# Kernel optimization log

Hardware: AMD Instinct MI355X
Metric: run time of the kernel (lower is better)

## Reference

```python
import jax, jax.numpy as jnp
import numpy as np

D_MODEL, H, D_FF = 512, 8, 2048
B, S = 2, 2048
EPS = 1e-6


def _layernorm(x, alpha, beta):
    # Faithful to the torch module: unbiased std (ddof=1), eps added to STD,
    # scalar alpha/beta parameters.
    m = jnp.mean(x, axis=-1, keepdims=True)
    var = jnp.sum((x - m) ** 2, axis=-1, keepdims=True) / (x.shape[-1] - 1)
    std = jnp.sqrt(var)
    return alpha * (x - m) / (std + EPS) + beta


def _mha(x, mask, Wq, bq, Wk, bk, Wv, bv, Wo, bo):
    Bn, Sn, D = x.shape
    dk = D // H
    q = (x @ Wq + bq).reshape(Bn, Sn, H, dk).transpose(0, 2, 1, 3)  # [B,H,S,dk]
    k = (x @ Wk + bk).reshape(Bn, Sn, H, dk).transpose(0, 2, 1, 3)
    v = (x @ Wv + bv).reshape(Bn, Sn, H, dk).transpose(0, 2, 1, 3)
    scores = jnp.einsum('bhqd,bhkd->bhqk', q, k) / jnp.sqrt(jnp.float32(dk))
    scores = jnp.where(mask == 0, -jnp.inf, scores)  # mask [B,1,1,S] broadcasts
    attn = jax.nn.softmax(scores, axis=-1)
    out = jnp.einsum('bhqk,bhkd->bhqd', attn, v)
    out = out.transpose(0, 2, 1, 3).reshape(Bn, Sn, D)
    return out @ Wo + bo


def _ffn(x, W1, b1, W2, b2):
    return jax.nn.relu(x @ W1 + b1) @ W2 + b2


def setup_inputs() -> dict:
    key = jax.random.key(0)
    ks = jax.random.split(key, 12)
    sd = 1.0 / np.sqrt(D_MODEL)
    sdf = 1.0 / np.sqrt(D_FF)
    inp = {
        'x': jax.random.normal(ks[0], (B, S, D_MODEL), jnp.float32),
        'src_mask': jnp.ones((B, 1, 1, S), jnp.int32),
        'Wq': jax.random.normal(ks[1], (D_MODEL, D_MODEL), jnp.float32) * sd,
        'bq': jnp.zeros((D_MODEL,), jnp.float32),
        'Wk': jax.random.normal(ks[2], (D_MODEL, D_MODEL), jnp.float32) * sd,
        'bk': jnp.zeros((D_MODEL,), jnp.float32),
        'Wv': jax.random.normal(ks[3], (D_MODEL, D_MODEL), jnp.float32) * sd,
        'bv': jnp.zeros((D_MODEL,), jnp.float32),
        'Wo': jax.random.normal(ks[4], (D_MODEL, D_MODEL), jnp.float32) * sd,
        'bo': jnp.zeros((D_MODEL,), jnp.float32),
        'W1': jax.random.normal(ks[5], (D_MODEL, D_FF), jnp.float32) * sd,
        'b1': jnp.zeros((D_FF,), jnp.float32),
        'W2': jax.random.normal(ks[6], (D_FF, D_MODEL), jnp.float32) * sdf,
        'b2': jnp.zeros((D_MODEL,), jnp.float32),
        'alpha1': jnp.ones((1,), jnp.float32),
        'beta1': jnp.zeros((1,), jnp.float32),
        'alpha2': jnp.ones((1,), jnp.float32),
        'beta2': jnp.zeros((1,), jnp.float32),
    }
    return inp


def reference(x, src_mask, Wq, bq, Wk, bk, Wv, bv, Wo, bo,
              W1, b1, W2, b2, alpha1, beta1, alpha2, beta2):
    # SkipConnection 0: x + dropout(MHA(LN(x)))  (dropout=0 -> identity)
    h1 = _layernorm(x, alpha1, beta1)
    x = x + _mha(h1, src_mask, Wq, bq, Wk, bk, Wv, bv, Wo, bo)
    # SkipConnection 1: x + dropout(FFN(LN(x)))
    h2 = _layernorm(x, alpha2, beta2)
    x = x + _ffn(h2, W1, b1, W2, b2)
    return x
```

## Files before the change

kernel.cpp:

```cpp
#include <hip/hip_runtime.h>
#include <hip/hip_bf16.h>

typedef __hip_bfloat16 bf16;
typedef __attribute__((ext_vector_type(8))) short s8v;
typedef __attribute__((ext_vector_type(4))) float f32x4;

#define DM 512
#define NH 8
#define DKH 64
#define DFF 2048
#define NB 2
#define NS 2048
#define NR (NB*NS)
#define LN_EPS 1e-6f
#define NEG_BIG (-1e30f)
#define LDQKV (3*DM)
#define SM_SHIFT (-6.0f)
#define PART_ELEMS (NB*NH*NS*DKH)

#define MFMA_B16(a,b,c) __builtin_amdgcn_mfma_f32_16x16x32_bf16(a,b,c,0,0,0)

#define GLOAD16(g, l) __builtin_amdgcn_global_load_lds( \
    (const __attribute__((address_space(1))) void*)(g), \
    (__attribute__((address_space(3))) void*)(l), 16, 0, 0)

__device__ __forceinline__ float us2f(unsigned int u){ return __uint_as_float(u << 16); }
__device__ __forceinline__ float b2f(bf16 v){ return __bfloat162float(v); }
__device__ __forceinline__ float ldf(const float* p){ return *p; }
__device__ __forceinline__ float ldf(const bf16* p){ return __bfloat162float(*p); }
__device__ __forceinline__ void stf(float* p, float v){ *p = v; }
__device__ __forceinline__ void stf(bf16* p, float v){ *p = __float2bfloat16(v); }
__device__ __forceinline__ unsigned short f2bu(float f){
  bf16 b = __float2bfloat16(f);
  return *reinterpret_cast<unsigned short*>(&b);
}

template<int N> __device__ __forceinline__ void waitcnt_vm(){
  if constexpr(N==0)      asm volatile("s_waitcnt vmcnt(0)" ::: "memory");
  else if constexpr(N==2) asm volatile("s_waitcnt vmcnt(2)" ::: "memory");
  else if constexpr(N==3) asm volatile("s_waitcnt vmcnt(3)" ::: "memory");
  else if constexpr(N==4) asm volatile("s_waitcnt vmcnt(4)" ::: "memory");
  else if constexpr(N==6) asm volatile("s_waitcnt vmcnt(6)" ::: "memory");
  else if constexpr(N==8) asm volatile("s_waitcnt vmcnt(8)" ::: "memory");
}

__device__ __forceinline__ int swz(int row, int colbyte){
  return ((row<<7) + colbyte) ^ ((row&7)<<4);
}

__device__ __forceinline__ float wsum(float v){
#pragma unroll
  for(int o=32;o>0;o>>=1) v += __shfl_down(v,o,64);
  return v;
}

__device__ __forceinline__ void stage_tile(char* lds, const bf16* g, int ld, int R, int tid){
  int wave = tid>>6, lane = tid&63;
  int nch = R*8;
  for(int c0 = wave*64; c0 < nch; c0 += 256){
    int c = c0 + lane;
    int row = c>>3;
    int blk = (c&7) ^ (row&7);
    GLOAD16(g + (size_t)row*ld + blk*8, lds + c0*16);
  }
}
__device__ __forceinline__ s8v read_frag(const char* lds, int row, int col){
  return *reinterpret_cast<const s8v*>(lds + swz(row, col<<1));
}

template<typename TI>
__global__ __launch_bounds__(256) void ln_kernel(const TI* __restrict__ x,
    bf16* __restrict__ out, const float* __restrict__ ap, const float* __restrict__ bp){
  __shared__ float s1[4], s2[4];
  int row = blockIdx.x, tid = threadIdx.x;
  const TI* xr = x + (size_t)row*DM;
  float v0 = ldf(xr+tid), v1 = ldf(xr+tid+256);
  float s = wsum(v0+v1);
  float q = wsum(v0*v0+v1*v1);
  int wid = tid>>6, lane = tid&63;
  if(lane==0){ s1[wid]=s; s2[wid]=q; }
  __syncthreads();
  float S = s1[0]+s1[1]+s1[2]+s1[3];
  float Q = s2[0]+s2[1]+s2[2]+s2[3];
  float mean = S*(1.f/DM);
  float var  = (Q - (float)DM*mean*mean)*(1.f/(DM-1));
  float sd   = sqrtf(fmaxf(var,0.f));
  float sc = (*ap)/(sd+LN_EPS);
  float b = *bp;
  bf16* orow = out + (size_t)row*DM;
  orow[tid]     = __float2bfloat16((v0-mean)*sc + b);
  orow[tid+256] = __float2bfloat16((v1-mean)*sc + b);
}

__global__ __launch_bounds__(256) void transpose_all(
    const float* __restrict__ Wq, const float* __restrict__ Wk,
    const float* __restrict__ Wv, const float* __restrict__ Wo,
    const float* __restrict__ W1, const float* __restrict__ W2,
    bf16* __restrict__ WTqkv, bf16* __restrict__ WTo,
    bf16* __restrict__ WT1, bf16* __restrict__ WT2){
  __shared__ float t[64][65];
  int tb = blockIdx.x;
  const float* W; bf16* WT; int K, N, nx;
  if(tb < 192){
    int w = tb>>6; tb &= 63;
    W = (w==0)?Wq:(w==1)?Wk:Wv; WT = WTqkv + w*512*512; K=512; N=512; nx=8;
  } else if(tb < 256){ tb -= 192; W=Wo; WT=WTo; K=512; N=512; nx=8; }
  else if(tb < 512){ tb -= 256; W=W1; WT=WT1; K=512; N=2048; nx=32; }
  else { tb -= 512; W=W2; WT=WT2; K=2048; N=512; nx=8; }
  int n0 = (tb % nx)*64, k0 = (tb / nx)*64;
  int tid = threadIdx.x;
  int rr = tid>>6, cc = tid&63;
#pragma unroll
  for(int r=rr;r<64;r+=4) t[r][cc] = W[(size_t)(k0+r)*N + n0+cc];
  __syncthreads();
#pragma unroll
  for(int r=rr;r<64;r+=4) WT[(size_t)(n0+r)*K + k0+cc] = __float2bfloat16(t[cc][r]);
}

__global__ __launch_bounds__(256) void transpose_v(const bf16* __restrict__ Vg,
    bf16* __restrict__ VT){
  __shared__ float t[64][65];
  int tid = threadIdx.x;
  int s0 = blockIdx.x*64; int bh = blockIdx.y;
  int b = bh>>3, h = bh&7;
  int rr = tid>>6, cc = tid&63;
#pragma unroll
  for(int r=rr;r<64;r+=4)
    t[r][cc] = b2f(Vg[((size_t)(b*NS + s0+r))*LDQKV + h*DKH + cc]);
  __syncthreads();
  int kp = (cc&15)*4 + (cc>>4);
#pragma unroll
  for(int r=rr;r<64;r+=4)
    VT[((size_t)bh*DKH + r)*NS + s0 + kp] = __float2bfloat16(t[cc][r]);
}

template<int BM, int BN, int RELU, int QKVSEL, typename TR, typename TO>
__global__ __launch_bounds__(256) void mfma_gemm(
    const bf16* __restrict__ A, const bf16* __restrict__ WT,
    const float* __restrict__ bias0, const float* __restrict__ bias1,
    const float* __restrict__ bias2,
    const TR* __restrict__ resid, TO* __restrict__ out, int M, int N, int K){
  constexpr int NW = BN/2, NF = NW/16, MI = (BM+31)/32, WRS = BM/2;
  constexpr int LOADS = BM/32 + BN/32;
  __shared__ char lA[2][BM*128];
  __shared__ char lB[2][BN*128];
  int tid = threadIdx.x, wave = tid>>6, lane = tid&63;
  int m0 = blockIdx.x*BM, n0 = blockIdx.y*BN;
  int wr = wave>>1, wc = wave&1;
  int g = lane>>4, li = lane&15;
  f32x4 acc[MI][NF] = {};
  stage_tile(lA[0], A + (size_t)m0*K, K, BM, tid);
  stage_tile(lB[0], WT + (size_t)n0*K, K, BN, tid);
  int NT = K>>6;
  int cur = 0;
  for(int t=0; t<NT; ++t, cur^=1){
    if(t+1 < NT){
      stage_tile(lA[cur^1], A + (size_t)m0*K + (t+1)*64, K, BM, tid);
      stage_tile(lB[cur^1], WT + (size_t)n0*K + (t+1)*64, K, BN, tid);
      waitcnt_vm<LOADS>();
    } else {
      waitcnt_vm<0>();
    }
    __builtin_amdgcn_sched_barrier(0);
    __builtin_amdgcn_s_barrier();
    __builtin_amdgcn_sched_barrier(0);
#pragma unroll
    for(int kk=0; kk<2; kk++){
      s8v af[MI], bfr[NF];
#pragma unroll
      for(int mi=0;mi<MI;mi++) af[mi] = read_frag(lA[cur], wr*WRS+mi*16+li, kk*32+g*8);
#pragma unroll
      for(int ni=0;ni<NF;ni++) bfr[ni] = read_frag(lB[cur], wc*NW+ni*16+li, kk*32+g*8);
#pragma unroll
      for(int mi=0;mi<MI;mi++)
#pragma unroll
        for(int ni=0;ni<NF;ni++)
          acc[mi][ni] = MFMA_B16(af[mi], bfr[ni], acc[mi][ni]);
    }
    __builtin_amdgcn_sched_barrier(0);
    __builtin_amdgcn_s_barrier();
  }
#pragma unroll
  for(int mi=0;mi<MI;mi++)
#pragma unroll
  for(int ni=0;ni<NF;ni++){
    int row = m0 + wr*WRS + mi*16 + g*4;
    int col = n0 + wc*NW + ni*16 + li;
    const float* bp = bias0;
    if(QKVSEL) bp = (col<512)? bias0 : (col<1024)? (bias1-512) : (bias2-1024);
    float bb = bp[col];
#pragma unroll
    for(int r=0;r<4;r++){
      float v = acc[mi][ni][r] + bb;
      if(RELU) v = fmaxf(v, 0.f);
      size_t off = (size_t)(row+r)*N + col;
      if(resid) v += ldf(resid+off);
      stf(out+off, v);
    }
  }
}

__global__ __launch_bounds__(256,4) void flash_attn(
    const bf16* __restrict__ QKV, const bf16* __restrict__ VT,
    const int* __restrict__ mask, bf16* __restrict__ partA,
    bf16* __restrict__ partB, float* __restrict__ lbuf){
  __shared__ char lK[2][64*128];
  __shared__ char lV[2][64*128];
  __shared__ char lP[4][16*128];
  int tid = threadIdx.x, wave = tid>>6, lane = tid&63;
  int bid = blockIdx.x;
  int xcd = bid & 7, u = bid >> 3;
  int q0 = (u & 31)*64;
  int bhk = xcd + 8*(u>>5);
  int h = bhk & 7, kh = (bhk>>3)&1, b = bhk>>4;
  int kbase = kh*(NS/2);
  int g = lane>>4, li = lane&15;
  const bf16* Qg  = QKV + ((size_t)b*NS + q0)*LDQKV + h*DKH;
  const bf16* Kg  = QKV + ((size_t)b*NS + kbase)*LDQKV + DM + h*DKH;
  const bf16* VTg = VT + ((size_t)(b*NH + h))*DKH*NS + kbase;
  stage_tile(lK[0], Qg, LDQKV, 64, tid);
  __syncthreads();
  s8v qf0 = read_frag(lK[0], wave*16+li, g*8);
  s8v qf1 = read_frag(lK[0], wave*16+li, 32+g*8);
  __syncthreads();
  stage_tile(lK[0], Kg, LDQKV, 64, tid);
  stage_tile(lV[0], VTg, NS, 64, tid);
  unsigned long long mb = 0;
#pragma unroll 16
  for(int j=0;j<64;j++)
    mb |= (unsigned long long)(mask[b*NS + kbase + j*16 + li] != 0) << j;
  __syncthreads();
  f32x4 acc[4] = {};
  f32x4 acc_l = {};
  s8v ones;
#pragma unroll
  for(int j=0;j<8;j++) ones[j] = (short)0x3F80;
  char* lPw = lP[wave];

  auto compute = [&](int kt, int c){
    f32x4 S[4] = {};
#pragma unroll
    for(int kk=0;kk<2;kk++){
      s8v qf = kk ? qf1 : qf0;
      s8v kf[4];
#pragma unroll
      for(int ni=0;ni<4;ni++) kf[ni] = read_frag(lK[c], ni*16+li, kk*32+g*8);
#pragma unroll
      for(int ni=0;ni<4;ni++)
        S[ni] = MFMA_B16(qf, kf[ni], S[ni]);
    }
    int jb = kt>>4;
    float madd[4];
#pragma unroll
    for(int ni=0;ni<4;ni++)
      madd[ni] = ((mb>>(jb+ni))&1ull) ? SM_SHIFT : NEG_BIG;
#pragma unroll
    for(int r=0;r<4;r++){
      float e0 = __expf(fmaf(S[0][r], 0.125f, madd[0]));
      float e1 = __expf(fmaf(S[1][r], 0.125f, madd[1]));
      float e2 = __expf(fmaf(S[2][r], 0.125f, madd[2]));
      float e3 = __expf(fmaf(S[3][r], 0.125f, madd[3]));
      int row = g*4 + r;
      uint2 w;
      w.x = (unsigned int)f2bu(e0) | ((unsigned int)f2bu(e1)<<16);
      w.y = (unsigned int)f2bu(e2) | ((unsigned int)f2bu(e3)<<16);
      *reinterpret_cast<uint2*>(lPw + swz(row, li<<3)) = w;
    }
#pragma unroll
    for(int kk=0;kk<2;kk++){
      s8v pf = read_frag(lPw, li, kk*32+g*8);
      s8v vf[4];
#pragma unroll
      for(int nd=0;nd<4;nd++) vf[nd] = read_frag(lV[c], nd*16+li, kk*32+g*8);
#pragma unroll
      for(int nd=0;nd<4;nd++)
        acc[nd] = MFMA_B16(pf, vf[nd], acc[nd]);
      acc_l = MFMA_B16(pf, ones, acc_l);
    }
  };

  int cur = 0;
  for(int t=0; t<15; ++t, cur^=1){
    stage_tile(lK[cur^1], Kg + (size_t)(t+1)*64*LDQKV, LDQKV, 64, tid);
    stage_tile(lV[cur^1], VTg + (t+1)*64, NS, 64, tid);
    waitcnt_vm<4>();
    __builtin_amdgcn_sched_barrier(0);
    __builtin_amdgcn_s_barrier();
    __builtin_amdgcn_sched_barrier(0);
    compute(t*64, cur);
    __builtin_amdgcn_sched_barrier(0);
    __builtin_amdgcn_s_barrier();
  }
  waitcnt_vm<0>();
  __builtin_amdgcn_sched_barrier(0);
  __builtin_amdgcn_s_barrier();
  __builtin_amdgcn_sched_barrier(0);
  compute(15*64, cur);

  bf16* part = kh ? partB : partA;
  size_t qb = (size_t)(b*NH + h)*NS;
#pragma unroll
  for(int r=0;r<4;r++){
    int qrow = q0 + wave*16 + g*4 + r;
#pragma unroll
    for(int nd=0;nd<4;nd++)
      part[(qb + qrow)*DKH + nd*16 + li] = __float2bfloat16(acc[nd][r]);
    if(li==0)
      lbuf[((size_t)((b*NH+h)*2 + kh))*NS + qrow] = acc_l[r];
  }
}

__global__ __launch_bounds__(256) void combine_attn(const bf16* __restrict__ pA,
    const bf16* __restrict__ pB, const float* __restrict__ lbuf,
    bf16* __restrict__ cx){
  int e = blockIdx.x*256 + threadIdx.x;
  int idx = e*4;
  int d = idx & 63, q = (idx>>6)&(NS-1), h = (idx>>17)&7, b = idx>>20;
  uint2 ua = *reinterpret_cast<const uint2*>(pA+idx);
  uint2 ub = *reinterpret_cast<const uint2*>(pB+idx);
  float lA = lbuf[((size_t)((b*NH+h)*2+0))*NS + q];
  float lB = lbuf[((size_t)((b*NH+h)*2+1))*NS + q];
  float il = 1.f/(lA+lB);
  bf16* o = cx + ((size_t)(b*NS+q)*DM + h*DKH + d);
  o[0] = __float2bfloat16((us2f(ua.x&0xffffu)+us2f(ub.x&0xffffu))*il);
  o[1] = __float2bfloat16((us2f(ua.x>>16)+us2f(ub.x>>16))*il);
  o[2] = __float2bfloat16((us2f(ua.y&0xffffu)+us2f(ub.y&0xffffu))*il);
  o[3] = __float2bfloat16((us2f(ua.y>>16)+us2f(ub.y>>16))*il);
}

extern "C" void kernel_launch(void* const* d_in, const int* in_sizes, int n_in,
                              void* d_out, int out_size, void* d_ws, size_t ws_size,
                              hipStream_t stream){
  const float* x   = (const float*)d_in[0];
  const int* mask  = (const int*)d_in[1];
  const float* Wq = (const float*)d_in[2];
  const float* bq = (const float*)d_in[3];
  const float* Wk = (const float*)d_in[4];
  const float* bk = (const float*)d_in[5];
  const float* Wv = (const float*)d_in[6];
  const float* bv = (const float*)d_in[7];
  const float* Wo = (const float*)d_in[8];
  const float* bo = (const float*)d_in[9];
  const float* W1 = (const float*)d_in[10];
  const float* b1 = (const float*)d_in[11];
  const float* W2 = (const float*)d_in[12];
  const float* b2 = (const float*)d_in[13];
  const float* a1 = (const float*)d_in[14];
  const float* be1= (const float*)d_in[15];
  const float* a2 = (const float*)d_in[16];
  const float* be2= (const float*)d_in[17];

  char* ws = (char*)d_ws;
  bf16* h1    = (bf16*)(ws);
  bf16* accA  = (bf16*)(ws);
  bf16* WTqkv = (bf16*)(ws + (size_t)( 4<<20));
  bf16* WTo   = (bf16*)(ws + (size_t)(11<<19));
  bf16* WT1   = (bf16*)(ws + (size_t)( 8<<20));
  bf16* WT2   = (bf16*)(ws + (size_t)(10<<20));
  bf16* qkv   = (bf16*)(ws + (size_t)(12<<20));
  bf16* VT    = (bf16*)(ws + (size_t)(24<<20));
  bf16* cx    = (bf16*)(ws + (size_t)(24<<20));
  bf16* x1    = h1;
  bf16* h2    = (bf16*)(ws + (size_t)( 4<<20));
  bf16* mid   = qkv;
  float* lbuf = (float*)d_out;
  bf16* accB  = (bf16*)((char*)d_out + (1<<20));

  transpose_all<<<768,256,0,stream>>>(Wq,Wk,Wv,Wo,W1,W2, WTqkv,WTo,WT1,WT2);

  ln_kernel<float><<<NR,256,0,stream>>>(x, h1, a1, be1);
  mfma_gemm<128,64,0,1,float,bf16><<<dim3(32,24),256,0,stream>>>(
      h1, WTqkv, bq, bk, bv, (const float*)nullptr, qkv, NR, LDQKV, DM);
  transpose_v<<<dim3(32,16),256,0,stream>>>(qkv + 2*DM, VT);
  flash_attn<<<1024,256,0,stream>>>(qkv, VT, mask, accA, accB, lbuf);
  combine_attn<<<PART_ELEMS/1024,256,0,stream>>>(accA, accB, lbuf, cx);
  mfma_gemm<32,64,0,0,float,bf16><<<dim3(128,8),256,0,stream>>>(
      cx, WTo, bo, bo, bo, x, x1, NR, DM, DM);
  ln_kernel<bf16><<<NR,256,0,stream>>>(x1, h2, a2, be2);
  mfma_gemm<128,128,1,0,float,bf16><<<dim3(32,16),256,0,stream>>>(
      h2, WT1, b1, b1, b1, (const float*)nullptr, mid, NR, DFF, DM);
  mfma_gemm<32,64,0,0,bf16,float><<<dim3(128,8),256,0,stream>>>(
      mid, WT2, b2, b2, b2, x1, (float*)d_out, NR, DM, DFF);
}
```

Measured before the change: 130.6 us.

## Use 128-query attention blocks with 8 waves sharing K/V tiles, add setprio

The flash attention kernel now runs 512 threads per block, each block covering 128 query rows instead of 64, so every staged K/V tile in LDS is reused by twice as many waves and the total K/V global traffic is halved. The Q tile is staged across both K buffers, the per-wave P scratch grows to 8 slots, and the wait count is adjusted for fewer loads per thread. s_setprio is raised around the MFMA sections so that waves doing matrix work are favoured over those doing the exp stage. The cost is half as many blocks (512) and larger blocks, which may lower occupancy or load balance across CUs.

Measured after the change: 127.1 us. 2.7% less time.

```diff
diff --git a/kernel.cpp b/kernel.cpp
--- a/kernel.cpp
+++ b/kernel.cpp
@@ -54,14 +54,13 @@
   return v;
 }
 
+template<int NTHR>
 __device__ __forceinline__ void stage_tile(char* lds, const bf16* g, int ld, int R, int tid){
-  int wave = tid>>6, lane = tid&63;
   int nch = R*8;
-  for(int c0 = wave*64; c0 < nch; c0 += 256){
-    int c = c0 + lane;
+  for(int c = tid; c < nch; c += NTHR){
     int row = c>>3;
     int blk = (c&7) ^ (row&7);
-    GLOAD16(g + (size_t)row*ld + blk*8, lds + c0*16);
+    GLOAD16(g + (size_t)row*ld + blk*8, lds + c*16);
   }
 }
 __device__ __forceinline__ s8v read_frag(const char* lds, int row, int col){
@@ -149,14 +148,14 @@
   int wr = wave>>1, wc = wave&1;
   int g = lane>>4, li = lane&15;
   f32x4 acc[MI][NF] = {};
-  stage_tile(lA[0], A + (size_t)m0*K, K, BM, tid);
-  stage_tile(lB[0], WT + (size_t)n0*K, K, BN, tid);
+  stage_tile<256>(lA[0], A + (size_t)m0*K, K, BM, tid);
+  stage_tile<256>(lB[0], WT + (size_t)n0*K, K, BN, tid);
   int NT = K>>6;
   int cur = 0;
   for(int t=0; t<NT; ++t, cur^=1){
     if(t+1 < NT){
-      stage_tile(lA[cur^1], A + (size_t)m0*K + (t+1)*64, K, BM, tid);
-      stage_tile(lB[cur^1], WT + (size_t)n0*K + (t+1)*64, K, BN, tid);
+      stage_tile<256>(lA[cur^1], A + (size_t)m0*K + (t+1)*64, K, BM, tid);
+      stage_tile<256>(lB[cur^1], WT + (size_t)n0*K + (t+1)*64, K, BN, tid);
       waitcnt_vm<LOADS>();
     } else {
       waitcnt_vm<0>();
@@ -200,31 +199,31 @@
   }
 }
 
-__global__ __launch_bounds__(256,4) void flash_attn(
+__global__ __launch_bounds__(512,4) void flash_attn(
     const bf16* __restrict__ QKV, const bf16* __restrict__ VT,
     const int* __restrict__ mask, bf16* __restrict__ partA,
     bf16* __restrict__ partB, float* __restrict__ lbuf){
   __shared__ char lK[2][64*128];
   __shared__ char lV[2][64*128];
-  __shared__ char lP[4][16*128];
+  __shared__ char lP[8][16*128];
   int tid = threadIdx.x, wave = tid>>6, lane = tid&63;
   int bid = blockIdx.x;
   int xcd = bid & 7, u = bid >> 3;
-  int q0 = (u & 31)*64;
-  int bhk = xcd + 8*(u>>5);
+  int q0 = (u & 15)*128;
+  int bhk = xcd + 8*(u>>4);
   int h = bhk & 7, kh = (bhk>>3)&1, b = bhk>>4;
   int kbase = kh*(NS/2);
   int g = lane>>4, li = lane&15;
   const bf16* Qg  = QKV + ((size_t)b*NS + q0)*LDQKV + h*DKH;
   const bf16* Kg  = QKV + ((size_t)b*NS + kbase)*LDQKV + DM + h*DKH;
   const bf16* VTg = VT + ((size_t)(b*NH + h))*DKH*NS + kbase;
-  stage_tile(lK[0], Qg, LDQKV, 64, tid);
-  __syncthreads();
-  s8v qf0 = read_frag(lK[0], wave*16+li, g*8);
-  s8v qf1 = read_frag(lK[0], wave*16+li, 32+g*8);
-  __syncthreads();
-  stage_tile(lK[0], Kg, LDQKV, 64, tid);
-  stage_tile(lV[0], VTg, NS, 64, tid);
+  stage_tile<512>((char*)lK, Qg, LDQKV, 128, tid);
+  __syncthreads();
+  s8v qf0 = read_frag((char*)lK, wave*16+li, g*8);
+  s8v qf1 = read_frag((char*)lK, wave*16+li, 32+g*8);
+  __syncthreads();
+  stage_tile<512>(lK[0], Kg, LDQKV, 64, tid);
+  stage_tile<512>(lV[0], VTg, NS, 64, tid);
   unsigned long long mb = 0;
 #pragma unroll 16
   for(int j=0;j<64;j++)
@@ -239,6 +238,7 @@
 
   auto compute = [&](int kt, int c){
     f32x4 S[4] = {};
+    __builtin_amdgcn_s_setprio(1);
 #pragma unroll
     for(int kk=0;kk<2;kk++){
       s8v qf = kk ? qf1 : qf0;
@@ -249,6 +249,7 @@
       for(int ni=0;ni<4;ni++)
         S[ni] = MFMA_B16(qf, kf[ni], S[ni]);
     }
+    __builtin_amdgcn_s_setprio(0);
     int jb = kt>>4;
     float madd[4];
 #pragma unroll
@@ -266,6 +267,7 @@
       w.y = (unsigned int)f2bu(e2) | ((unsigned int)f2bu(e3)<<16);
       *reinterpret_cast<uint2*>(lPw + swz(row, li<<3)) = w;
     }
+    __builtin_amdgcn_s_setprio(1);
 #pragma unroll
     for(int kk=0;kk<2;kk++){
       s8v pf = read_frag(lPw, li, kk*32+g*8);
@@ -277,13 +279,14 @@
         acc[nd] = MFMA_B16(pf, vf[nd], acc[nd]);
       acc_l = MFMA_B16(pf, ones, acc_l);
     }
+    __builtin_amdgcn_s_setprio(0);
   };
 
   int cur = 0;
   for(int t=0; t<15; ++t, cur^=1){
-    stage_tile(lK[cur^1], Kg + (size_t)(t+1)*64*LDQKV, LDQKV, 64, tid);
-    stage_tile(lV[cur^1], VTg + (t+1)*64, NS, 64, tid);
-    waitcnt_vm<4>();
+    stage_tile<512>(lK[cur^1], Kg + (size_t)(t+1)*64*LDQKV, LDQKV, 64, tid);
+    stage_tile<512>(lV[cur^1], VTg + (t+1)*64, NS, 64, tid);
+    waitcnt_vm<2>();
     __builtin_amdgcn_sched_barrier(0);
     __builtin_amdgcn_s_barrier();
     __builtin_amdgcn_sched_barrier(0);
@@ -372,7 +375,7 @@
   mfma_gemm<128,64,0,1,float,bf16><<<dim3(32,24),256,0,stream>>>(
       h1, WTqkv, bq, bk, bv, (const float*)nullptr, qkv, NR, LDQKV, DM);
   transpose_v<<<dim3(32,16),256,0,stream>>>(qkv + 2*DM, VT);
-  flash_attn<<<1024,256,0,stream>>>(qkv, VT, mask, accA, accB, lbuf);
+  flash_attn<<<512,512,0,stream>>>(qkv, VT, mask, accA, accB, lbuf);
   combine_attn<<<PART_ELEMS/1024,256,0,stream>>>(accA, accB, lbuf, cx);
   mfma_gemm<32,64,0,0,float,bf16><<<dim3(128,8),256,0,stream>>>(
       cx, WTo, bo, bo, bo, x, x1, NR, DM, DM);
```
